# Kernel tuning notes

Hardware: AMD Instinct MI355X
Metric: run time of the kernel (lower is better)

Reference implementation:

```python
import jax, jax.numpy as jnp
import numpy as np

B, T, I, H, O = 64, 2048, 16, 256, 1


def _gru_layer(x, Wih, Whh, bih, bhh):
    # x: [B, T, in]; Wih: [3H, in]; Whh: [3H, H]
    xg = jnp.einsum('bti,gi->btg', x, Wih) + bih  # [B, T, 3H] precomputed input gates

    def step(h, xg_t):
        gh = h @ Whh.T + bhh  # [B, 3H]
        xr, xz, xn = jnp.split(xg_t, 3, axis=-1)
        hr, hz, hn = jnp.split(gh, 3, axis=-1)
        r = jax.nn.sigmoid(xr + hr)
        z = jax.nn.sigmoid(xz + hz)
        n = jnp.tanh(xn + r * hn)
        h_new = (1.0 - z) * n + z * h
        return h_new, h_new

    h0 = jnp.zeros((x.shape[0], Whh.shape[1]), dtype=x.dtype)
    _, hs = jax.lax.scan(step, h0, jnp.swapaxes(xg, 0, 1))  # [T, B, H]
    return jnp.swapaxes(hs, 0, 1)  # [B, T, H]


def setup_inputs() -> dict:
    key = jax.random.key(0)
    ks = jax.random.split(key, 8)

    def xavier(k, shape):
        fan_out, fan_in = shape
        lim = float(np.sqrt(6.0 / (fan_in + fan_out)))
        return jax.random.uniform(k, shape, jnp.float32, -lim, lim)

    return {
        'x': jax.random.normal(ks[0], (B, T, I), jnp.float32),
        'Wih0': xavier(ks[1], (3 * H, I)),
        'Whh0': xavier(ks[2], (3 * H, H)),
        'bih0': jnp.zeros((3 * H,), jnp.float32),
        'bhh0': jnp.zeros((3 * H,), jnp.float32),
        'Wih1': xavier(ks[3], (3 * H, H)),
        'Whh1': xavier(ks[4], (3 * H, H)),
        'bih1': jnp.zeros((3 * H,), jnp.float32),
        'bhh1': jnp.zeros((3 * H,), jnp.float32),
        'W1': xavier(ks[5], (H, H)),
        'b1': jnp.zeros((H,), jnp.float32),
        'W2': xavier(ks[6], (O, H)),
        'b2': jnp.zeros((O,), jnp.float32),
    }


def reference(x, Wih0, Whh0, bih0, bhh0, Wih1, Whh1, bih1, bhh1, W1, b1, W2, b2):
    h1 = _gru_layer(x, Wih0, Whh0, bih0, bhh0)    # layer 0: [B, T, H]
    h2 = _gru_layer(h1, Wih1, Whh1, bih1, bhh1)   # layer 1: [B, T, H]
    r = jax.nn.relu(jnp.einsum('bth,oh->bto', h2, W1) + b1)
    out = jnp.einsum('bth,oh->bto', r, W2) + b2
    return jax.nn.relu(out)  # final relu in forward, [B, T, O]
```

## Files before the change

### kernel.cpp

```cpp
#include <hip/hip_runtime.h>
#include <hip/hip_fp16.h>
#include <stdint.h>

#define B_ 64
#define T_ 2048
#define I_ 16
#define H_ 256
#define G_ 768

typedef _Float16 f16;
typedef _Float16 half2_t __attribute__((ext_vector_type(2)));
typedef uint32_t u32x4 __attribute__((ext_vector_type(4)));

__device__ __forceinline__ float fast_rcp(float x) {
#if __has_builtin(__builtin_amdgcn_rcpf)
    return __builtin_amdgcn_rcpf(x);
#else
    return 1.0f / x;
#endif
}
__device__ __forceinline__ float sigmoid_f(float x) {
    return fast_rcp(1.0f + __expf(-x));
}
__device__ __forceinline__ float tanh_f(float x) {
    float e = __expf(2.0f * x);
    return 1.0f - 2.0f * fast_rcp(e + 1.0f);
}

__device__ __forceinline__ float fdot2(uint32_t a, uint32_t b, float c) {
#if __has_builtin(__builtin_amdgcn_fdot2)
    return __builtin_amdgcn_fdot2(__builtin_bit_cast(half2_t, a),
                                  __builtin_bit_cast(half2_t, b), c, false);
#else
    half2_t ha = __builtin_bit_cast(half2_t, a), hb = __builtin_bit_cast(half2_t, b);
    return c + (float)ha.x * (float)hb.x + (float)ha.y * (float)hb.y;
#endif
}
__device__ __forceinline__ float dot_u4(u32x4 w, u32x4 h, float acc) {
    acc = fdot2(w.x, h.x, acc);
    acc = fdot2(w.y, h.y, acc);
    acc = fdot2(w.z, h.z, acc);
    acc = fdot2(w.w, h.w, acc);
    return acc;
}

__global__ __launch_bounds__(256) void cvt_weights(const float* __restrict__ whh0,
                                                   const float* __restrict__ whh1,
                                                   const float* __restrict__ wih1,
                                                   const float* __restrict__ w1,
                                                   uint32_t* __restrict__ out) {
    int idx = blockIdx.x * 256 + threadIdx.x;
    if (idx >= 327680) return;
    const float* s;
    if (idx < 196608) {
        const float* w = (idx < 98304) ? whh0 : whh1;
        int local = (idx < 98304) ? idx : idx - 98304;
        int row = local >> 7, kd = local & 127;
        s = w + (size_t)row * 256 + kd * 2;
    } else if (idx < 294912) {
        int local = idx - 196608;
        int u4 = local >> 2, d = local & 3;
        int k8 = u4 / 768, g = u4 - k8 * 768;
        s = wih1 + (size_t)g * 256 + k8 * 8 + d * 2;
    } else {
        int local = idx - 294912;
        int u4 = local >> 2, d = local & 3;
        int k8 = u4 >> 8, g = u4 & 255;
        s = w1 + (size_t)g * 256 + k8 * 8 + d * 2;
    }
    half2_t h;
    h.x = (f16)s[0];
    h.y = (f16)s[1];
    out[idx] = __builtin_bit_cast(uint32_t, h);
}


__device__ __forceinline__ void xg0_body(const float* __restrict__ x,
        const float* __restrict__ wih0, const float* __restrict__ bih0,
        float* __restrict__ xg, int t0, int C, int blk, char* smem) {
    float (*xs)[16] = (float(*)[16])smem;
    int tid = threadIdx.x;
    int m0 = blk * 64;
    if (tid < 256) {
        int r = tid >> 2, c4 = (tid & 3) * 4;
        int m = m0 + r;
        int b = m / C, tl = m - b * C;
        float4 v = *(const float4*)(x + (size_t)(b * T_ + t0 + tl) * I_ + c4);
        *(float4*)&xs[r][c4] = v;
    }
    __syncthreads();
    for (int g = tid; g < G_; g += 512) {
        const float4* wr = (const float4*)(wih0 + (size_t)g * I_);
        float4 w0 = wr[0], w1 = wr[1], w2 = wr[2], w3 = wr[3];
        float bias = bih0[g];
        float* outp = xg + (size_t)m0 * G_ + g;
        for (int m = 0; m < 64; ++m) {
            const float4* xr4 = (const float4*)xs[m];
            float4 a0 = xr4[0], a1 = xr4[1], a2 = xr4[2], a3 = xr4[3];
            float acc = bias;
            acc += a0.x*w0.x + a0.y*w0.y + a0.z*w0.z + a0.w*w0.w;
            acc += a1.x*w1.x + a1.y*w1.y + a1.z*w1.z + a1.w*w1.w;
            acc += a2.x*w2.x + a2.y*w2.y + a2.z*w2.z + a2.w*w2.w;
            acc += a3.x*w3.x + a3.y*w3.y + a3.z*w3.z + a3.w*w3.w;
            outp[(size_t)m * G_] = acc;
        }
    }
}

__device__ __forceinline__ void reg_body(const f16* __restrict__ h2,
        const uint32_t* __restrict__ w1T, const float* __restrict__ b1,
        const float* __restrict__ w2, const float* __restrict__ b2,
        float* __restrict__ out, int t0, int C, int lgC, int blk, char* smem) {
    u32x4 (*hs)[32] = (u32x4(*)[32])smem;
    float (*red)[4] = (float(*)[4])(smem + 32768);
    int tid = threadIdx.x;
    int m0 = blk * 64;
    const u32x4* hsrc = (const u32x4*)h2 + (size_t)m0 * 32;
    #pragma unroll
    for (int it = 0; it < 4; ++it) {
        int o = tid + it * 512;
        hs[o >> 5][o & 31] = hsrc[o];
    }
    __syncthreads();
    int gg = tid & 31, mg = tid >> 5;
    const u32x4* wt = (const u32x4*)w1T;
    float acc[8][4];
    #pragma unroll
    for (int i = 0; i < 8; ++i)
        #pragma unroll
        for (int r = 0; r < 4; ++r) acc[i][r] = 0.0f;
    for (int k8 = 0; k8 < 32; ++k8) {
        u32x4 w[8], h[4];
        #pragma unroll
        for (int i = 0; i < 8; ++i) w[i] = wt[(size_t)k8 * 256 + gg + 32 * i];
        #pragma unroll
        for (int r = 0; r < 4; ++r) h[r] = hs[mg * 4 + r][k8];
        #pragma unroll
        for (int i = 0; i < 8; ++i)
            #pragma unroll
            for (int r = 0; r < 4; ++r)
                acc[i][r] = dot_u4(w[i], h[r], acc[i][r]);
    }
    float pv[4] = {0, 0, 0, 0};
    #pragma unroll
    for (int i = 0; i < 8; ++i) {
        int g = gg + 32 * i;
        float bias = b1[g], w2g = w2[g];
        #pragma unroll
        for (int r = 0; r < 4; ++r)
            pv[r] += w2g * fmaxf(acc[i][r] + bias, 0.0f);
    }
    #pragma unroll
    for (int r = 0; r < 4; ++r) {
        pv[r] += __shfl_xor(pv[r], 1, 64);
        pv[r] += __shfl_xor(pv[r], 2, 64);
        pv[r] += __shfl_xor(pv[r], 4, 64);
        pv[r] += __shfl_xor(pv[r], 8, 64);
        pv[r] += __shfl_xor(pv[r], 16, 64);
    }
    if (gg == 0) {
        #pragma unroll
        for (int r = 0; r < 4; ++r) red[mg][r] = pv[r];
    }
    __syncthreads();
    if (tid < 64) {
        int m = m0 + tid;
        float v = fmaxf(red[tid >> 2][tid & 3] + b2[0], 0.0f);
        int b = m >> lgC, tl = m & (C - 1);
        out[(size_t)b * T_ + t0 + tl] = v;
    }
}

#define LOADROW(t, BASE) \
    u32x4 W##t##0 = wu[(BASE) + 0], W##t##1 = wu[(BASE) + 1], \
          W##t##2 = wu[(BASE) + 2], W##t##3 = wu[(BASE) + 3], \
          W##t##4 = wu[(BASE) + 4], W##t##5 = wu[(BASE) + 5], \
          W##t##6 = wu[(BASE) + 6], W##t##7 = wu[(BASE) + 7];

#define PINROW(t) asm volatile("" : \
    "+v"(W##t##0), "+v"(W##t##1), "+v"(W##t##2), "+v"(W##t##3), \
    "+v"(W##t##4), "+v"(W##t##5), "+v"(W##t##6), "+v"(W##t##7))

#define DOTU(u) { u32x4 hv = hp[u]; \
    a0 = dot_u4(W0##u, hv, a0); a1 = dot_u4(W1##u, hv, a1); \
    a2 = dot_u4(W2##u, hv, a2); a3 = dot_u4(W3##u, hv, a3); \
    a4 = dot_u4(W4##u, hv, a4); a5 = dot_u4(W5##u, hv, a5); }

__device__ __forceinline__ void rec_body(const uint32_t* __restrict__ whh,
        const float* __restrict__ bhh, const float* __restrict__ xg,
        f16* __restrict__ hout, float* __restrict__ state,
        int b, int C, char* smem) {
    uint32_t (*hq)[4][36] = (uint32_t(*)[4][36])smem;

    int tid = threadIdx.x;
    int g = tid >> 2, q = tid & 3;

    const u32x4* wu = (const u32x4*)whh;
    LOADROW(0, (g)       * 32 + q * 8)
    LOADROW(1, (128 + g) * 32 + q * 8)
    LOADROW(2, (256 + g) * 32 + q * 8)
    LOADROW(3, (384 + g) * 32 + q * 8)
    LOADROW(4, (512 + g) * 32 + q * 8)
    LOADROW(5, (640 + g) * 32 + q * 8)

    int j = g + (q << 7);
    float h_old = 0.0f, bhr = 0.0f, bhz = 0.0f, bhn = 0.0f;
    if (q < 2) {
        h_old = state[b * 256 + j];
        bhr = bhh[j]; bhz = bhh[256 + j]; bhn = bhh[512 + j];
        ((f16*)&hq[0][j >> 6][0])[j & 63] = (f16)h_old;
    }
    __syncthreads();

    const float* xgt = xg + (size_t)b * C * G_;
    f16* hob = hout + (size_t)b * C * H_;

    for (int tl = 0; tl < C; ++tl) {
        PINROW(0); PINROW(1); PINROW(2); PINROW(3); PINROW(4); PINROW(5);

        int p = tl & 1;
        float xr = 0, xz = 0, xn = 0;
        if (q < 2) { xr = xgt[j]; xz = xgt[256 + j]; xn = xgt[512 + j]; }

        const u32x4* hp = (const u32x4*)&hq[p][q][0];
        float a0 = 0, a1 = 0, a2 = 0, a3 = 0, a4 = 0, a5 = 0;
        DOTU(0) DOTU(1) DOTU(2) DOTU(3) DOTU(4) DOTU(5) DOTU(6) DOTU(7)

        a0 += __shfl_xor(a0, 1, 64); a0 += __shfl_xor(a0, 2, 64);
        a1 += __shfl_xor(a1, 1, 64); a1 += __shfl_xor(a1, 2, 64);
        a2 += __shfl_xor(a2, 1, 64); a2 += __shfl_xor(a2, 2, 64);
        a3 += __shfl_xor(a3, 1, 64); a3 += __shfl_xor(a3, 2, 64);
        a4 += __shfl_xor(a4, 1, 64); a4 += __shfl_xor(a4, 2, 64);
        a5 += __shfl_xor(a5, 1, 64); a5 += __shfl_xor(a5, 2, 64);

        if (q < 2) {
            float sumR = q ? a1 : a0;
            float sumZ = q ? a3 : a2;
            float sumN = q ? a5 : a4;
            float r = sigmoid_f(xr + sumR + bhr);
            float z = sigmoid_f(xz + sumZ + bhz);
            float n = tanh_f(xn + r * (sumN + bhn));
            h_old = z * (h_old - n) + n;
            f16 hh = (f16)h_old;
            hob[(size_t)tl * H_ + j] = hh;
            ((f16*)&hq[p ^ 1][j >> 6][0])[j & 63] = hh;
        }
        __syncthreads();
        xgt += G_;
    }
    if (q < 2) state[b * 256 + j] = h_old;
}

__global__ __launch_bounds__(512, 2) void fused_step(int i, int nC, int C, int lgC,
        const float* __restrict__ x,
        const float* __restrict__ wih0, const float* __restrict__ bih0,
        const uint32_t* __restrict__ whh0, const float* __restrict__ bhh0,
        const uint32_t* __restrict__ whh1, const float* __restrict__ bhh1,
        const uint32_t* __restrict__ w1T, const float* __restrict__ b1,
        const float* __restrict__ w2, const float* __restrict__ b2,
        float* __restrict__ xg0a, float* __restrict__ xg0b,
        float* __restrict__ xg1b,
        f16* __restrict__ h1,
        f16* __restrict__ h2a, f16* __restrict__ h2b,
        float* __restrict__ st0, float* __restrict__ st1,
        float* __restrict__ out) {
    __shared__ __align__(16) char smem[33024];
    int blk = blockIdx.x;
    if (blk < 128) {
        const uint32_t* whh; const float* bhh; const float* xgp; f16* hout; float* st; int b;
        if (blk < 64) {
            if (i >= nC) return;
            whh = whh0; bhh = bhh0; xgp = (i & 1) ? xg0b : xg0a;
            hout = h1; st = st0; b = blk;
        } else {
            if (i < 1) return;
            whh = whh1; bhh = bhh1; xgp = xg1b;
            hout = ((i - 1) & 1) ? h2b : h2a; st = st1; b = blk - 64;
        }
        rec_body(whh, bhh, xgp, hout, st, b, C, smem);
    } else if (blk < 128 + C) {
        if (i + 1 >= nC) return;
        xg0_body(x, wih0, bih0, ((i + 1) & 1) ? xg0b : xg0a, (i + 1) * C, C, blk - 128, smem);
    } else {
        if (i < 2) return;
        reg_body((i & 1) ? h2b : h2a, w1T, b1, w2, b2, out, (i - 2) * C, C, lgC,
                 blk - 128 - C, smem);
    }
}

__global__ __launch_bounds__(512, 2) void xg0_stand(const float* __restrict__ x,
        const float* __restrict__ wih0, const float* __restrict__ bih0,
        float* __restrict__ xg, int t0, int C) {
    __shared__ __align__(16) char smem[4096];
    xg0_body(x, wih0, bih0, xg, t0, C, blockIdx.x, smem);
}

__global__ __launch_bounds__(512, 2) void reg_stand(const f16* __restrict__ h2,
        const uint32_t* __restrict__ w1T, const float* __restrict__ b1,
        const float* __restrict__ w2, const float* __restrict__ b2,
        float* __restrict__ out, int t0, int C, int lgC) {
    __shared__ __align__(16) char smem[33024];
    reg_body(h2, w1T, b1, w2, b2, out, t0, C, lgC, blockIdx.x, smem);
}

__global__ __launch_bounds__(256) void xg1_kernel(const f16* __restrict__ h1,
        const uint32_t* __restrict__ wih1T, const float* __restrict__ bih1,
        float* __restrict__ xg, int C) {
    __shared__ u32x4 hs[64][32];
    int tid = threadIdx.x;
    int m0 = blockIdx.x * 64;
    int gbase = blockIdx.y * 256;
    const u32x4* hsrc = (const u32x4*)h1 + (size_t)m0 * 32;
    #pragma unroll
    for (int it = 0; it < 8; ++it) {
        int o = tid + it * 256;
        hs[o >> 5][o & 31] = hsrc[o];
    }
    __syncthreads();
    int gg = tid & 31, mg = tid >> 5;
    const u32x4* wt = (const u32x4*)wih1T;
    float acc[8][8];
    #pragma unroll
    for (int i = 0; i < 8; ++i)
        #pragma unroll
        for (int r = 0; r < 8; ++r) acc[i][r] = 0.0f;
    for (int k8 = 0; k8 < 32; ++k8) {
        u32x4 w[8], h[8];
        #pragma unroll
        for (int i = 0; i < 8; ++i) w[i] = wt[(size_t)k8 * 768 + gbase + gg + 32 * i];
        #pragma unroll
        for (int r = 0; r < 8; ++r) h[r] = hs[mg * 8 + r][k8];
        #pragma unroll
        for (int i = 0; i < 8; ++i)
            #pragma unroll
            for (int r = 0; r < 8; ++r)
                acc[i][r] = dot_u4(w[i], h[r], acc[i][r]);
    }
    #pragma unroll
    for (int i = 0; i < 8; ++i) {
        int g = gbase + gg + 32 * i;
        float bias = bih1[g];
        #pragma unroll
        for (int r = 0; r < 8; ++r)
            xg[(size_t)(m0 + mg * 8 + r) * G_ + g] = acc[i][r] + bias;
    }
}

extern "C" void kernel_launch(void* const* d_in, const int* in_sizes, int n_in,
                              void* d_out, int out_size, void* d_ws, size_t ws_size,
                              hipStream_t stream) {
    const float* x    = (const float*)d_in[0];
    const float* Wih0 = (const float*)d_in[1];
    const float* Whh0 = (const float*)d_in[2];
    const float* bih0 = (const float*)d_in[3];
    const float* bhh0 = (const float*)d_in[4];
    const float* Wih1 = (const float*)d_in[5];
    const float* Whh1 = (const float*)d_in[6];
    const float* bih1 = (const float*)d_in[7];
    const float* bhh1 = (const float*)d_in[8];
    const float* W1   = (const float*)d_in[9];
    const float* b1   = (const float*)d_in[10];
    const float* W2   = (const float*)d_in[11];
    const float* b2   = (const float*)d_in[12];
    float* out = (float*)d_out;

    char* ws = (char*)d_ws;
    uint32_t* wcvt = (uint32_t*)ws;
    const uint32_t* whh0_16 = wcvt;
    const uint32_t* whh1_16 = wcvt + 98304;
    const uint32_t* wih1T   = wcvt + 196608;
    const uint32_t* w1T     = wcvt + 294912;
    float* state0 = (float*)(ws + 1310720);
    float* state1 = (float*)(ws + 1310720 + 65536);
    size_t fixed = 1310720 + 2 * 65536;

    int C = 512;
    while (C > 32 && fixed + (size_t)C * 688128 > ws_size) C >>= 1;
    int lgC = 0; while ((1 << lgC) < C) lgC++;
    int nC = T_ / C;

    char* p = ws + fixed;
    float* xg0_buf[2];
    xg0_buf[0] = (float*)p;  p += (size_t)C * 196608;
    xg0_buf[1] = (float*)p;  p += (size_t)C * 196608;
    float* xg1_buf = (float*)p; p += (size_t)C * 196608;
    f16* h1_buf = (f16*)p;   p += (size_t)C * 32768;
    f16* h2_buf[2];
    h2_buf[0] = (f16*)p;     p += (size_t)C * 32768;
    h2_buf[1] = (f16*)p;

    cvt_weights<<<1280, 256, 0, stream>>>(Whh0, Whh1, Wih1, W1, wcvt);
    hipMemsetAsync(state0, 0, 2 * 65536, stream);
    xg0_stand<<<C, 512, 0, stream>>>(x, Wih0, bih0, xg0_buf[0], 0, C);

    for (int i = 0; i <= nC; ++i) {
        fused_step<<<128 + 2 * C, 512, 0, stream>>>(i, nC, C, lgC,
            x, Wih0, bih0, whh0_16, bhh0, whh1_16, bhh1, w1T, b1, W2, b2,
            xg0_buf[0], xg0_buf[1], xg1_buf, h1_buf, h2_buf[0], h2_buf[1],
            state0, state1, out);
        if (i < nC)
            xg1_kernel<<<dim3(C, 3), 256, 0, stream>>>(h1_buf, wih1T, bih1, xg1_buf, C);
    }
    reg_stand<<<C, 512, 0, stream>>>(h2_buf[(nC - 1) & 1], w1T, b1, W2, b2, out,
                                     (nC - 1) * C, C, lgC);
}
```

Baseline: 3.325 ms.

## Use one thread per hidden unit in recurrent GRU kernel with 256-thread blocks

The recurrent step used 512 threads, each computing a quarter-row partial dot product followed by cross-lane shuffle reductions. It now uses 256 threads, each owning a full hidden unit and holding all three gate rows (96 u32x4 values) in registers, which removes the shuffle reductions and the idle lanes. Whh is re-laid out transposed to match, the block size drops to 256 across all fused kernels, and the xg0 and regressor bodies are retiled (3 gate passes, 8 rows per thread). The cost is a serial 256-element dot product per thread, very high register pressure, and half as many waves to hide latency in each step.

Measured after the change: 6.352 ms. +91.0%, slower.

```diff
diff --git a/kernel.cpp b/kernel.cpp
--- a/kernel.cpp
+++ b/kernel.cpp
@@ -55,8 +55,9 @@
     if (idx < 196608) {
         const float* w = (idx < 98304) ? whh0 : whh1;
         int local = (idx < 98304) ? idx : idx - 98304;
-        int row = local >> 7, kd = local & 127;
-        s = w + (size_t)row * 256 + kd * 2;
+        int u4 = local >> 2, d = local & 3;
+        int k8 = u4 / 768, row = u4 - k8 * 768;
+        s = w + (size_t)row * 256 + k8 * 8 + d * 2;
     } else if (idx < 294912) {
         int local = idx - 196608;
         int u4 = local >> 2, d = local & 3;
@@ -81,7 +82,7 @@
     float (*xs)[16] = (float(*)[16])smem;
     int tid = threadIdx.x;
     int m0 = blk * 64;
-    if (tid < 256) {
+    {
         int r = tid >> 2, c4 = (tid & 3) * 4;
         int m = m0 + r;
         int b = m / C, tl = m - b * C;
@@ -89,7 +90,9 @@
         *(float4*)&xs[r][c4] = v;
     }
     __syncthreads();
-    for (int g = tid; g < G_; g += 512) {
+    #pragma unroll
+    for (int gi = 0; gi < 3; ++gi) {
+        int g = gi * 256 + tid;
         const float4* wr = (const float4*)(wih0 + (size_t)g * I_);
         float4 w0 = wr[0], w1 = wr[1], w2 = wr[2], w3 = wr[3];
         float bias = bih0[g];
@@ -112,46 +115,48 @@
         const float* __restrict__ w2, const float* __restrict__ b2,
         float* __restrict__ out, int t0, int C, int lgC, int blk, char* smem) {
     u32x4 (*hs)[32] = (u32x4(*)[32])smem;
-    float (*red)[4] = (float(*)[4])(smem + 32768);
+    float (*red)[8] = (float(*)[8])(smem + 32768);
     int tid = threadIdx.x;
     int m0 = blk * 64;
     const u32x4* hsrc = (const u32x4*)h2 + (size_t)m0 * 32;
     #pragma unroll
-    for (int it = 0; it < 4; ++it) {
-        int o = tid + it * 512;
+    for (int it = 0; it < 8; ++it) {
+        int o = tid + it * 256;
         hs[o >> 5][o & 31] = hsrc[o];
     }
     __syncthreads();
     int gg = tid & 31, mg = tid >> 5;
     const u32x4* wt = (const u32x4*)w1T;
-    float acc[8][4];
+    float acc[8][8];
     #pragma unroll
     for (int i = 0; i < 8; ++i)
         #pragma unroll
-        for (int r = 0; r < 4; ++r) acc[i][r] = 0.0f;
+        for (int r = 0; r < 8; ++r) acc[i][r] = 0.0f;
     for (int k8 = 0; k8 < 32; ++k8) {
-        u32x4 w[8], h[4];
+        u32x4 w[8], h[8];
         #pragma unroll
         for (int i = 0; i < 8; ++i) w[i] = wt[(size_t)k8 * 256 + gg + 32 * i];
         #pragma unroll
-        for (int r = 0; r < 4; ++r) h[r] = hs[mg * 4 + r][k8];
+        for (int r = 0; r < 8; ++r) h[r] = hs[mg * 8 + r][k8];
         #pragma unroll
         for (int i = 0; i < 8; ++i)
             #pragma unroll
-            for (int r = 0; r < 4; ++r)
+            for (int r = 0; r < 8; ++r)
                 acc[i][r] = dot_u4(w[i], h[r], acc[i][r]);
     }
-    float pv[4] = {0, 0, 0, 0};
+    float pv[8];
+    #pragma unroll
+    for (int r = 0; r < 8; ++r) pv[r] = 0.0f;
     #pragma unroll
     for (int i = 0; i < 8; ++i) {
         int g = gg + 32 * i;
         float bias = b1[g], w2g = w2[g];
         #pragma unroll
-        for (int r = 0; r < 4; ++r)
+        for (int r = 0; r < 8; ++r)
             pv[r] += w2g * fmaxf(acc[i][r] + bias, 0.0f);
     }
     #pragma unroll
-    for (int r = 0; r < 4; ++r) {
+    for (int r = 0; r < 8; ++r) {
         pv[r] += __shfl_xor(pv[r], 1, 64);
         pv[r] += __shfl_xor(pv[r], 2, 64);
         pv[r] += __shfl_xor(pv[r], 4, 64);
@@ -160,102 +165,73 @@
     }
     if (gg == 0) {
         #pragma unroll
-        for (int r = 0; r < 4; ++r) red[mg][r] = pv[r];
+        for (int r = 0; r < 8; ++r) red[mg][r] = pv[r];
     }
     __syncthreads();
     if (tid < 64) {
         int m = m0 + tid;
-        float v = fmaxf(red[tid >> 2][tid & 3] + b2[0], 0.0f);
+        float v = fmaxf(red[tid >> 3][tid & 7] + b2[0], 0.0f);
         int b = m >> lgC, tl = m & (C - 1);
         out[(size_t)b * T_ + t0 + tl] = v;
     }
 }
 
-#define LOADROW(t, BASE) \
-    u32x4 W##t##0 = wu[(BASE) + 0], W##t##1 = wu[(BASE) + 1], \
-          W##t##2 = wu[(BASE) + 2], W##t##3 = wu[(BASE) + 3], \
-          W##t##4 = wu[(BASE) + 4], W##t##5 = wu[(BASE) + 5], \
-          W##t##6 = wu[(BASE) + 6], W##t##7 = wu[(BASE) + 7];
-
-#define PINROW(t) asm volatile("" : \
-    "+v"(W##t##0), "+v"(W##t##1), "+v"(W##t##2), "+v"(W##t##3), \
-    "+v"(W##t##4), "+v"(W##t##5), "+v"(W##t##6), "+v"(W##t##7))
-
-#define DOTU(u) { u32x4 hv = hp[u]; \
-    a0 = dot_u4(W0##u, hv, a0); a1 = dot_u4(W1##u, hv, a1); \
-    a2 = dot_u4(W2##u, hv, a2); a3 = dot_u4(W3##u, hv, a3); \
-    a4 = dot_u4(W4##u, hv, a4); a5 = dot_u4(W5##u, hv, a5); }
-
-__device__ __forceinline__ void rec_body(const uint32_t* __restrict__ whh,
+__device__ __forceinline__ void rec_body(const uint32_t* __restrict__ whhT,
         const float* __restrict__ bhh, const float* __restrict__ xg,
         f16* __restrict__ hout, float* __restrict__ state,
         int b, int C, char* smem) {
-    uint32_t (*hq)[4][36] = (uint32_t(*)[4][36])smem;
-
-    int tid = threadIdx.x;
-    int g = tid >> 2, q = tid & 3;
-
-    const u32x4* wu = (const u32x4*)whh;
-    LOADROW(0, (g)       * 32 + q * 8)
-    LOADROW(1, (128 + g) * 32 + q * 8)
-    LOADROW(2, (256 + g) * 32 + q * 8)
-    LOADROW(3, (384 + g) * 32 + q * 8)
-    LOADROW(4, (512 + g) * 32 + q * 8)
-    LOADROW(5, (640 + g) * 32 + q * 8)
-
-    int j = g + (q << 7);
-    float h_old = 0.0f, bhr = 0.0f, bhz = 0.0f, bhn = 0.0f;
-    if (q < 2) {
-        h_old = state[b * 256 + j];
-        bhr = bhh[j]; bhz = bhh[256 + j]; bhn = bhh[512 + j];
-        ((f16*)&hq[0][j >> 6][0])[j & 63] = (f16)h_old;
-    }
+    u32x4 (*hq)[32] = (u32x4(*)[32])smem;
+    int j = threadIdx.x;
+
+    const u32x4* wu = (const u32x4*)whhT;
+    u32x4 W0[32], W1[32], W2[32];
+    #pragma unroll
+    for (int k8 = 0; k8 < 32; ++k8) {
+        W0[k8] = wu[(size_t)k8 * 768 + j];
+        W1[k8] = wu[(size_t)k8 * 768 + 256 + j];
+        W2[k8] = wu[(size_t)k8 * 768 + 512 + j];
+    }
+
+    float h_old = state[b * 256 + j];
+    float bhr = bhh[j], bhz = bhh[256 + j], bhn = bhh[512 + j];
+    ((f16*)&hq[0][0])[j] = (f16)h_old;
     __syncthreads();
 
     const float* xgt = xg + (size_t)b * C * G_;
     f16* hob = hout + (size_t)b * C * H_;
 
     for (int tl = 0; tl < C; ++tl) {
-        PINROW(0); PINROW(1); PINROW(2); PINROW(3); PINROW(4); PINROW(5);
-
         int p = tl & 1;
-        float xr = 0, xz = 0, xn = 0;
-        if (q < 2) { xr = xgt[j]; xz = xgt[256 + j]; xn = xgt[512 + j]; }
-
-        const u32x4* hp = (const u32x4*)&hq[p][q][0];
-        float a0 = 0, a1 = 0, a2 = 0, a3 = 0, a4 = 0, a5 = 0;
-        DOTU(0) DOTU(1) DOTU(2) DOTU(3) DOTU(4) DOTU(5) DOTU(6) DOTU(7)
-
-        a0 += __shfl_xor(a0, 1, 64); a0 += __shfl_xor(a0, 2, 64);
-        a1 += __shfl_xor(a1, 1, 64); a1 += __shfl_xor(a1, 2, 64);
-        a2 += __shfl_xor(a2, 1, 64); a2 += __shfl_xor(a2, 2, 64);
-        a3 += __shfl_xor(a3, 1, 64); a3 += __shfl_xor(a3, 2, 64);
-        a4 += __shfl_xor(a4, 1, 64); a4 += __shfl_xor(a4, 2, 64);
-        a5 += __shfl_xor(a5, 1, 64); a5 += __shfl_xor(a5, 2, 64);
-
-        if (q < 2) {
-            float sumR = q ? a1 : a0;
-            float sumZ = q ? a3 : a2;
-            float sumN = q ? a5 : a4;
-            float r = sigmoid_f(xr + sumR + bhr);
-            float z = sigmoid_f(xz + sumZ + bhz);
-            float n = tanh_f(xn + r * (sumN + bhn));
-            h_old = z * (h_old - n) + n;
-            f16 hh = (f16)h_old;
-            hob[(size_t)tl * H_ + j] = hh;
-            ((f16*)&hq[p ^ 1][j >> 6][0])[j & 63] = hh;
+        float xr = xgt[j], xz = xgt[256 + j], xn = xgt[512 + j];
+
+        float aR = 0.0f, aZ = 0.0f, aN = 0.0f;
+        #pragma unroll
+        for (int k8 = 0; k8 < 32; ++k8) {
+            u32x4 hv = hq[p][k8];
+            aR = dot_u4(W0[k8], hv, aR);
+            aZ = dot_u4(W1[k8], hv, aZ);
+            aN = dot_u4(W2[k8], hv, aN);
         }
+        float r = sigmoid_f(xr + aR + bhr);
+        float z = sigmoid_f(xz + aZ + bhz);
+        float n = tanh_f(xn + r * (aN + bhn));
+        h_old = z * (h_old - n) + n;
+        f16 hh = (f16)h_old;
+        hob[(size_t)tl * H_ + j] = hh;
+        ((f16*)&hq[p ^ 1][0])[j] = hh;
         __syncthreads();
         xgt += G_;
     }
-    if (q < 2) state[b * 256 + j] = h_old;
-}
-
-__global__ __launch_bounds__(512, 2) void fused_step(int i, int nC, int C, int lgC,
+    state[b * 256 + j] = h_old;
+}
+
+__global__ __launch_bounds__(256)
+__attribute__((amdgpu_waves_per_eu(1, 1)))
+void fused_step(int i, int nC, int C, int lgC,
         const float* __restrict__ x,
         const float* __restrict__ wih0, const float* __restrict__ bih0,
-        const uint32_t* __restrict__ whh0, const float* __restrict__ bhh0,
-        const uint32_t* __restrict__ whh1, const float* __restrict__ bhh1,
+        const uint32_t* __restrict__ whh0T, const float* __restrict__ bhh0,
+        const uint32_t* __restrict__ whh1T, const float* __restrict__ bhh1,
         const uint32_t* __restrict__ w1T, const float* __restrict__ b1,
         const float* __restrict__ w2, const float* __restrict__ b2,
         float* __restrict__ xg0a, float* __restrict__ xg0b,
@@ -270,11 +246,11 @@
         const uint32_t* whh; const float* bhh; const float* xgp; f16* hout; float* st; int b;
         if (blk < 64) {
             if (i >= nC) return;
-            whh = whh0; bhh = bhh0; xgp = (i & 1) ? xg0b : xg0a;
+            whh = whh0T; bhh = bhh0; xgp = (i & 1) ? xg0b : xg0a;
             hout = h1; st = st0; b = blk;
         } else {
             if (i < 1) return;
-            whh = whh1; bhh = bhh1; xgp = xg1b;
+            whh = whh1T; bhh = bhh1; xgp = xg1b;
             hout = ((i - 1) & 1) ? h2b : h2a; st = st1; b = blk - 64;
         }
         rec_body(whh, bhh, xgp, hout, st, b, C, smem);
@@ -288,14 +264,23 @@
     }
 }
 
-__global__ __launch_bounds__(512, 2) void xg0_stand(const float* __restrict__ x,
+__global__ __launch_bounds__(256)
+__attribute__((amdgpu_waves_per_eu(1, 1)))
+void rec_stand(const uint32_t* __restrict__ whhT, const float* __restrict__ bhh,
+        const float* __restrict__ xg, f16* __restrict__ hout,
+        float* __restrict__ state, int C) {
+    __shared__ __align__(16) char smem[1024];
+    rec_body(whhT, bhh, xg, hout, state, blockIdx.x, C, smem);
+}
+
+__global__ __launch_bounds__(256) void xg0_stand(const float* __restrict__ x,
         const float* __restrict__ wih0, const float* __restrict__ bih0,
         float* __restrict__ xg, int t0, int C) {
     __shared__ __align__(16) char smem[4096];
     xg0_body(x, wih0, bih0, xg, t0, C, blockIdx.x, smem);
 }
 
-__global__ __launch_bounds__(512, 2) void reg_stand(const f16* __restrict__ h2,
+__global__ __launch_bounds__(256) void reg_stand(const f16* __restrict__ h2,
         const uint32_t* __restrict__ w1T, const float* __restrict__ b1,
         const float* __restrict__ w2, const float* __restrict__ b2,
         float* __restrict__ out, int t0, int C, int lgC) {
@@ -366,10 +351,10 @@
 
     char* ws = (char*)d_ws;
     uint32_t* wcvt = (uint32_t*)ws;
-    const uint32_t* whh0_16 = wcvt;
-    const uint32_t* whh1_16 = wcvt + 98304;
-    const uint32_t* wih1T   = wcvt + 196608;
-    const uint32_t* w1T     = wcvt + 294912;
+    const uint32_t* whh0T = wcvt;
+    const uint32_t* whh1T = wcvt + 98304;
+    const uint32_t* wih1T = wcvt + 196608;
+    const uint32_t* w1T   = wcvt + 294912;
     float* state0 = (float*)(ws + 1310720);
     float* state1 = (float*)(ws + 1310720 + 65536);
     size_t fixed = 1310720 + 2 * 65536;
@@ -391,16 +376,16 @@
 
     cvt_weights<<<1280, 256, 0, stream>>>(Whh0, Whh1, Wih1, W1, wcvt);
     hipMemsetAsync(state0, 0, 2 * 65536, stream);
-    xg0_stand<<<C, 512, 0, stream>>>(x, Wih0, bih0, xg0_buf[0], 0, C);
+    xg0_stand<<<C, 256, 0, stream>>>(x, Wih0, bih0, xg0_buf[0], 0, C);
 
     for (int i = 0; i <= nC; ++i) {
-        fused_step<<<128 + 2 * C, 512, 0, stream>>>(i, nC, C, lgC,
-            x, Wih0, bih0, whh0_16, bhh0, whh1_16, bhh1, w1T, b1, W2, b2,
+        fused_step<<<128 + 2 * C, 256, 0, stream>>>(i, nC, C, lgC,
+            x, Wih0, bih0, whh0T, bhh0, whh1T, bhh1, w1T, b1, W2, b2,
             xg0_buf[0], xg0_buf[1], xg1_buf, h1_buf, h2_buf[0], h2_buf[1],
             state0, state1, out);
         if (i < nC)
             xg1_kernel<<<dim3(C, 3), 256, 0, stream>>>(h1_buf, wih1T, bih1, xg1_buf, C);
     }
-    reg_stand<<<C, 512, 0, stream>>>(h2_buf[(nC - 1) & 1], w1T, b1, W2, b2, out,
+    reg_stand<<<C, 256, 0, stream>>>(h2_buf[(nC - 1) & 1], w1T, b1, W2, b2, out,
                                      (nC - 1) * C, C, lgC);
 }
```

## Restructure GRU recurrence: stream R/Z weights from global, keep N rows in LDS

Applied to the files above, without the earlier changes.

The recurrent kernel previously held all Whh rows in registers across 4 threads per output pair. Now each output j is handled by two threads. The R and Z gate weights are re-read from global memory (L1/L2) every timestep in a coalesced reordered layout, and the N gate weights are staged into 128KB of swizzled LDS. The weight conversion kernel is changed to emit that reordered layout, and fused_step switches to dynamic shared memory with relaxed launch bounds. This is meant to ease register pressure and raise occupancy, but it adds per-step global/cache traffic and a large LDS footprint that allows only one block per CU.

New measurement: 3.634 ms. 1.09x slower.

```diff
diff --git a/kernel.cpp b/kernel.cpp
--- a/kernel.cpp
+++ b/kernel.cpp
@@ -7,6 +7,8 @@
 #define I_ 16
 #define H_ 256
 #define G_ 768
+
+#define REC_SMEM 132096
 
 typedef _Float16 f16;
 typedef _Float16 half2_t __attribute__((ext_vector_type(2)));
@@ -54,9 +56,20 @@
     const float* s;
     if (idx < 196608) {
         const float* w = (idx < 98304) ? whh0 : whh1;
-        int local = (idx < 98304) ? idx : idx - 98304;
-        int row = local >> 7, kd = local & 127;
-        s = w + (size_t)row * 256 + kd * 2;
+        int lidx = (idx < 98304) ? idx : idx - 98304;
+        int u4 = lidx >> 2, d = lidx & 3;
+        int row, halfoff;
+        if (u4 < 16384) {
+            int u = u4 >> 9, tid = u4 & 511;
+            int j = tid >> 1, hf = tid & 1;
+            row = (u < 16 ? 0 : 256) + j;
+            halfoff = hf * 128 + (u & 15) * 8;
+        } else {
+            int l2 = u4 - 16384;
+            row = 512 + (l2 >> 5);
+            halfoff = (l2 & 31) * 8;
+        }
+        s = w + (size_t)row * 256 + halfoff + d * 2;
     } else if (idx < 294912) {
         int local = idx - 196608;
         int u4 = local >> 2, d = local & 3;
@@ -171,87 +184,74 @@
     }
 }
 
-#define LOADROW(t, BASE) \
-    u32x4 W##t##0 = wu[(BASE) + 0], W##t##1 = wu[(BASE) + 1], \
-          W##t##2 = wu[(BASE) + 2], W##t##3 = wu[(BASE) + 3], \
-          W##t##4 = wu[(BASE) + 4], W##t##5 = wu[(BASE) + 5], \
-          W##t##6 = wu[(BASE) + 6], W##t##7 = wu[(BASE) + 7];
-
-#define PINROW(t) asm volatile("" : \
-    "+v"(W##t##0), "+v"(W##t##1), "+v"(W##t##2), "+v"(W##t##3), \
-    "+v"(W##t##4), "+v"(W##t##5), "+v"(W##t##6), "+v"(W##t##7))
-
-#define DOTU(u) { u32x4 hv = hp[u]; \
-    a0 = dot_u4(W0##u, hv, a0); a1 = dot_u4(W1##u, hv, a1); \
-    a2 = dot_u4(W2##u, hv, a2); a3 = dot_u4(W3##u, hv, a3); \
-    a4 = dot_u4(W4##u, hv, a4); a5 = dot_u4(W5##u, hv, a5); }
-
 __device__ __forceinline__ void rec_body(const uint32_t* __restrict__ whh,
         const float* __restrict__ bhh, const float* __restrict__ xg,
         f16* __restrict__ hout, float* __restrict__ state,
         int b, int C, char* smem) {
-    uint32_t (*hq)[4][36] = (uint32_t(*)[4][36])smem;
-
     int tid = threadIdx.x;
-    int g = tid >> 2, q = tid & 3;
-
-    const u32x4* wu = (const u32x4*)whh;
-    LOADROW(0, (g)       * 32 + q * 8)
-    LOADROW(1, (128 + g) * 32 + q * 8)
-    LOADROW(2, (256 + g) * 32 + q * 8)
-    LOADROW(3, (384 + g) * 32 + q * 8)
-    LOADROW(4, (512 + g) * 32 + q * 8)
-    LOADROW(5, (640 + g) * 32 + q * 8)
-
-    int j = g + (q << 7);
+    int j = tid >> 1, hf = tid & 1;
+    const u32x4* wb = (const u32x4*)whh;
+    u32x4 (*hq)[32] = (u32x4(*)[32])(smem + 131072);
+
+    const u32x4* n_rm = wb + 16384;
+    #pragma unroll
+    for (int it = 0; it < 16; ++it) {
+        int idx = it * 512 + tid;
+        int row = idx >> 5, u = idx & 31;
+        u32x4 v = n_rm[idx];
+        *(u32x4*)(smem + row * 512 + ((u * 16) ^ ((row & 15) << 4))) = v;
+    }
+
     float h_old = 0.0f, bhr = 0.0f, bhz = 0.0f, bhn = 0.0f;
-    if (q < 2) {
+    if (hf == 0) {
         h_old = state[b * 256 + j];
         bhr = bhh[j]; bhz = bhh[256 + j]; bhn = bhh[512 + j];
-        ((f16*)&hq[0][j >> 6][0])[j & 63] = (f16)h_old;
+        ((f16*)&hq[0][0])[j] = (f16)h_old;
     }
     __syncthreads();
 
     const float* xgt = xg + (size_t)b * C * G_;
     f16* hob = hout + (size_t)b * C * H_;
+    const char* nrow = smem + j * 512;
+    int jsw = (j & 15) << 4;
 
     for (int tl = 0; tl < C; ++tl) {
-        PINROW(0); PINROW(1); PINROW(2); PINROW(3); PINROW(4); PINROW(5);
-
         int p = tl & 1;
         float xr = 0, xz = 0, xn = 0;
-        if (q < 2) { xr = xgt[j]; xz = xgt[256 + j]; xn = xgt[512 + j]; }
-
-        const u32x4* hp = (const u32x4*)&hq[p][q][0];
-        float a0 = 0, a1 = 0, a2 = 0, a3 = 0, a4 = 0, a5 = 0;
-        DOTU(0) DOTU(1) DOTU(2) DOTU(3) DOTU(4) DOTU(5) DOTU(6) DOTU(7)
-
-        a0 += __shfl_xor(a0, 1, 64); a0 += __shfl_xor(a0, 2, 64);
-        a1 += __shfl_xor(a1, 1, 64); a1 += __shfl_xor(a1, 2, 64);
-        a2 += __shfl_xor(a2, 1, 64); a2 += __shfl_xor(a2, 2, 64);
-        a3 += __shfl_xor(a3, 1, 64); a3 += __shfl_xor(a3, 2, 64);
-        a4 += __shfl_xor(a4, 1, 64); a4 += __shfl_xor(a4, 2, 64);
-        a5 += __shfl_xor(a5, 1, 64); a5 += __shfl_xor(a5, 2, 64);
-
-        if (q < 2) {
-            float sumR = q ? a1 : a0;
-            float sumZ = q ? a3 : a2;
-            float sumN = q ? a5 : a4;
-            float r = sigmoid_f(xr + sumR + bhr);
-            float z = sigmoid_f(xz + sumZ + bhz);
-            float n = tanh_f(xn + r * (sumN + bhn));
+        if (hf == 0) { xr = xgt[j]; xz = xgt[256 + j]; xn = xgt[512 + j]; }
+
+        const u32x4* hp = &hq[p][hf * 16];
+        float aR = 0.0f, aZ = 0.0f, aN = 0.0f;
+        #pragma unroll
+        for (int u = 0; u < 16; ++u) {
+            u32x4 hv = hp[u];
+            u32x4 wr = wb[u * 512 + tid];
+            u32x4 wz = wb[(16 + u) * 512 + tid];
+            u32x4 wn = *(const u32x4*)(nrow + ((hf * 256 + u * 16) ^ jsw));
+            aR = dot_u4(wr, hv, aR);
+            aZ = dot_u4(wz, hv, aZ);
+            aN = dot_u4(wn, hv, aN);
+        }
+        aR += __shfl_xor(aR, 1, 64);
+        aZ += __shfl_xor(aZ, 1, 64);
+        aN += __shfl_xor(aN, 1, 64);
+
+        if (hf == 0) {
+            float r = sigmoid_f(xr + aR + bhr);
+            float z = sigmoid_f(xz + aZ + bhz);
+            float n = tanh_f(xn + r * (aN + bhn));
             h_old = z * (h_old - n) + n;
             f16 hh = (f16)h_old;
             hob[(size_t)tl * H_ + j] = hh;
-            ((f16*)&hq[p ^ 1][j >> 6][0])[j & 63] = hh;
+            ((f16*)&hq[p ^ 1][0])[j] = hh;
         }
         __syncthreads();
         xgt += G_;
     }
-    if (q < 2) state[b * 256 + j] = h_old;
-}
-
-__global__ __launch_bounds__(512, 2) void fused_step(int i, int nC, int C, int lgC,
+    if (hf == 0) state[b * 256 + j] = h_old;
+}
+
+__global__ __launch_bounds__(512) void fused_step(int i, int nC, int C, int lgC,
         const float* __restrict__ x,
         const float* __restrict__ wih0, const float* __restrict__ bih0,
         const uint32_t* __restrict__ whh0, const float* __restrict__ bhh0,
@@ -264,7 +264,7 @@
         f16* __restrict__ h2a, f16* __restrict__ h2b,
         float* __restrict__ st0, float* __restrict__ st1,
         float* __restrict__ out) {
-    __shared__ __align__(16) char smem[33024];
+    extern __shared__ __align__(16) char smem[];
     int blk = blockIdx.x;
     if (blk < 128) {
         const uint32_t* whh; const float* bhh; const float* xgp; f16* hout; float* st; int b;
@@ -288,14 +288,14 @@
     }
 }
 
-__global__ __launch_bounds__(512, 2) void xg0_stand(const float* __restrict__ x,
+__global__ __launch_bounds__(512) void xg0_stand(const float* __restrict__ x,
         const float* __restrict__ wih0, const float* __restrict__ bih0,
         float* __restrict__ xg, int t0, int C) {
     __shared__ __align__(16) char smem[4096];
     xg0_body(x, wih0, bih0, xg, t0, C, blockIdx.x, smem);
 }
 
-__global__ __launch_bounds__(512, 2) void reg_stand(const f16* __restrict__ h2,
+__global__ __launch_bounds__(512) void reg_stand(const f16* __restrict__ h2,
         const uint32_t* __restrict__ w1T, const float* __restrict__ b1,
         const float* __restrict__ w2, const float* __restrict__ b2,
         float* __restrict__ out, int t0, int C, int lgC) {
@@ -364,12 +364,15 @@
     const float* b2   = (const float*)d_in[12];
     float* out = (float*)d_out;
 
+    hipFuncSetAttribute(reinterpret_cast<const void*>(fused_step),
+                        hipFuncAttributeMaxDynamicSharedMemorySize, REC_SMEM);
+
     char* ws = (char*)d_ws;
     uint32_t* wcvt = (uint32_t*)ws;
-    const uint32_t* whh0_16 = wcvt;
-    const uint32_t* whh1_16 = wcvt + 98304;
-    const uint32_t* wih1T   = wcvt + 196608;
-    const uint32_t* w1T     = wcvt + 294912;
+    const uint32_t* whh0c = wcvt;
+    const uint32_t* whh1c = wcvt + 98304;
+    const uint32_t* wih1T = wcvt + 196608;
+    const uint32_t* w1T   = wcvt + 294912;
     float* state0 = (float*)(ws + 1310720);
     float* state1 = (float*)(ws + 1310720 + 65536);
     size_t fixed = 1310720 + 2 * 65536;
@@ -394,8 +397,8 @@
     xg0_stand<<<C, 512, 0, stream>>>(x, Wih0, bih0, xg0_buf[0], 0, C);
 
     for (int i = 0; i <= nC; ++i) {
-        fused_step<<<128 + 2 * C, 512, 0, stream>>>(i, nC, C, lgC,
-            x, Wih0, bih0, whh0_16, bhh0, whh1_16, bhh1, w1T, b1, W2, b2,
+        fused_step<<<128 + 2 * C, 512, REC_SMEM, stream>>>(i, nC, C, lgC,
+            x, Wih0, bih0, whh0c, bhh0, whh1c, bhh1, w1T, b1, W2, b2,
             xg0_buf[0], xg0_buf[1], xg1_buf, h1_buf, h2_buf[0], h2_buf[1],
             state0, state1, out);
         if (i < nC)
```
